# Optimization experiments

Measured on AMD Instinct MI355X. Metric: run time of the kernel, lower is better.

Reference implementation:

```python
import jax, jax.numpy as jnp
import numpy as np

IH, IW, HEADS, DIM_HEAD = 32, 32, 8, 48
N = IH * IW
SCALE = DIM_HEAD ** -0.5
EPS = 1e-5


def _relative_index():
    # static precompute of relative distance indices, shape [N, N] int32
    yy, xx = np.meshgrid(np.arange(IH), np.arange(IW), indexing='ij')
    coords = np.stack([yy.ravel(), xx.ravel()])  # [2, N]
    rel = coords[:, :, None] - coords[:, None, :]  # [2, N, N]
    dist = np.ceil(np.sqrt(rel[0] ** 2 + rel[1] ** 2)).astype(np.int32)
    return jnp.asarray(dist)

REL_INDEX = _relative_index()


def _layernorm(x, w, b):
    mu = jnp.mean(x, axis=-1, keepdims=True)
    var = jnp.var(x, axis=-1, keepdims=True)
    return (x - mu) * jax.lax.rsqrt(var + EPS) * w + b


def setup_inputs() -> dict:
    key = jax.random.key(0)
    ks = jax.random.split(key, 8)
    d, inner, hid = 384, HEADS * DIM_HEAD, 1536
    return {
        'x': jax.random.normal(ks[0], (16, IH, IW, d), jnp.float32),
        'ln1_w': jnp.ones((d,), jnp.float32),
        'ln1_b': jnp.zeros((d,), jnp.float32),
        'w_qkv': jax.random.normal(ks[1], (d, 3 * inner), jnp.float32) * (d ** -0.5),
        'bias_table': jax.random.normal(ks[2], (45, HEADS), jnp.float32) * 0.02,
        'w_out': jax.random.normal(ks[3], (inner, d), jnp.float32) * (inner ** -0.5),
        'b_out': jnp.zeros((d,), jnp.float32),
        'ln2_w': jnp.ones((d,), jnp.float32),
        'ln2_b': jnp.zeros((d,), jnp.float32),
        'w1': jax.random.normal(ks[4], (d, hid), jnp.float32) * (d ** -0.5),
        'b1': jnp.zeros((hid,), jnp.float32),
        'w2': jax.random.normal(ks[5], (hid, d), jnp.float32) * (hid ** -0.5),
        'b2': jnp.zeros((d,), jnp.float32),
    }


def reference(x, ln1_w, ln1_b, w_qkv, bias_table, w_out, b_out,
              ln2_w, ln2_b, w1, b1, w2, b2):
    b = x.shape[0]
    xt = x.reshape(b, N, -1)  # b (ih iw) c

    # --- attention branch (PreNorm) ---
    h = _layernorm(xt, ln1_w, ln1_b)
    qkv = h @ w_qkv  # [b, N, 3*inner]
    q, k, v = jnp.split(qkv, 3, axis=-1)
    q = q.reshape(b, N, HEADS, DIM_HEAD).transpose(0, 2, 1, 3)
    k = k.reshape(b, N, HEADS, DIM_HEAD).transpose(0, 2, 1, 3)
    v = v.reshape(b, N, HEADS, DIM_HEAD).transpose(0, 2, 1, 3)
    dots = jnp.einsum('bhnd,bhmd->bhnm', q, k) * SCALE
    rel_bias = bias_table[REL_INDEX]  # [N, N, heads] gather
    dots = dots + rel_bias.transpose(2, 0, 1)[None]  # [1, h, N, N]
    attn = jax.nn.softmax(dots, axis=-1)
    out = jnp.einsum('bhnm,bhmd->bhnd', attn, v)
    out = out.transpose(0, 2, 1, 3).reshape(b, N, HEADS * DIM_HEAD)
    out = out @ w_out + b_out
    xt = xt + out

    # --- FFN branch (PreNorm) ---
    h = _layernorm(xt, ln2_w, ln2_b)
    h = jax.nn.gelu(h @ w1 + b1, approximate=False) @ w2 + b2
    xt = xt + h
    return xt.reshape(x.shape)
```

## Files before the change

kernel.cpp:

```cpp
#include <hip/hip_runtime.h>
#include <hip/hip_bf16.h>
#include <math.h>

typedef __bf16 bf16;
typedef __bf16 bf16x8 __attribute__((ext_vector_type(8)));
typedef __bf16 bf16x4 __attribute__((ext_vector_type(4)));
typedef float  f32x4  __attribute__((ext_vector_type(4)));

#define D_MODEL 384
#define HID     1536
#define NSEQ    1024
#define ROWS    16384
#define HEADS   8
#define DH      48
#define SCALE   0.14433756729740643f
#define MFIX    8.0f
#define BTAB_N  3969
#define BTAB_P  3972
#define KVT     4608
#define QP_BH   (NSEQ * DH)
#define KP_BH   (16 * KVT)

__device__ __forceinline__ void gload16(const void* g, void* l) {
    __builtin_amdgcn_global_load_lds((const __attribute__((address_space(1))) void*)g,
                                     (__attribute__((address_space(3))) void*)l, 16, 0, 0);
}

__device__ __forceinline__ float fast_gelu(float x) {
    float u = 0.7978845608f * fmaf(0.044715f * x * x, x, x);
    float e = __expf(2.f * u);
    float t = 1.f - 2.f * __builtin_amdgcn_rcpf(e + 1.f);
    return 0.5f * x * (1.f + t);
}

__global__ __launch_bounds__(256)
void bias_prep_kernel(const float* __restrict__ bias_table, float* __restrict__ Btab)
{
    int idx = blockIdx.x * 256 + threadIdx.x;
    if (idx >= BTAB_N) return;
    int dy = idx / 63 - 31, dx = idx % 63 - 31;
    int s2 = dy * dy + dx * dx;
    int r = (int)ceilf(sqrtf((float)s2));
    while (r * r < s2) ++r;
    while (r > 0 && (r - 1) * (r - 1) >= s2) --r;
#pragma unroll
    for (int h = 0; h < HEADS; ++h)
        Btab[h * BTAB_P + idx] = bias_table[r * HEADS + h] - MFIX;
}

__global__ __launch_bounds__(256)
void pack_init_kernel(bf16* __restrict__ Kp, bf16* __restrict__ Vp)
{
    const int bid = blockIdx.x, tid = threadIdx.x;
    if (bid < 512) {
        int row = bid * 256 + tid;
        bf16x8 z = {};
        bf16* p = Kp + (size_t)row * 72 + 48;
        *(bf16x8*)(p) = z;  *(bf16x8*)(p + 8) = z;  *(bf16x8*)(p + 16) = z;
    } else {
        int idx = (bid - 512) * 256 + tid;
        int tile = idx >> 4, rr = idx & 15;
        bf16 o = (bf16)1.f;
        bf16x8 ones = {o, o, o, o, o, o, o, o};
        bf16* p = Vp + (size_t)tile * KVT + (48 + rr) * 72;
#pragma unroll
        for (int c = 0; c < 9; ++c) *(bf16x8*)(p + c * 8) = ones;
    }
}

__global__ __launch_bounds__(256)
void wtrans_kernel(const float* __restrict__ in, bf16* __restrict__ out, int K, int N)
{
    __shared__ float T[64][65];
    const int k0 = blockIdx.y * 64, n0 = blockIdx.x * 64;
    const int rr = threadIdx.x >> 4, rc = threadIdx.x & 15;
#pragma unroll
    for (int i = 0; i < 4; ++i) {
        float4 v = *(const float4*)(in + (size_t)(k0 + rr + i * 16) * N + n0 + rc * 4);
        T[rr + i * 16][rc * 4 + 0] = v.x;  T[rr + i * 16][rc * 4 + 1] = v.y;
        T[rr + i * 16][rc * 4 + 2] = v.z;  T[rr + i * 16][rc * 4 + 3] = v.w;
    }
    __syncthreads();
#pragma unroll
    for (int i = 0; i < 4; ++i) {
        int n = rr + i * 16, kc = rc * 4;
        bf16x4 o;
        o[0] = (bf16)T[kc + 0][n];  o[1] = (bf16)T[kc + 1][n];
        o[2] = (bf16)T[kc + 2][n];  o[3] = (bf16)T[kc + 3][n];
        *(bf16x4*)(out + (size_t)(n0 + n) * K + k0 + kc) = o;
    }
}

__global__ __launch_bounds__(64)
void ln_kernel(const float* __restrict__ x, const float* __restrict__ w,
               const float* __restrict__ b, bf16* __restrict__ out)
{
    int row  = blockIdx.x;
    int lane = threadIdx.x;
    const float* xr = x + (size_t)row * D_MODEL;

    float v[6], s = 0.f, ss = 0.f;
#pragma unroll
    for (int i = 0; i < 6; ++i) {
        v[i] = xr[lane + i * 64];
        s  += v[i];
        ss += v[i] * v[i];
    }
#pragma unroll
    for (int off = 32; off; off >>= 1) {
        s  += __shfl_xor(s,  off);
        ss += __shfl_xor(ss, off);
    }
    float mu   = s * (1.f / D_MODEL);
    float var  = ss * (1.f / D_MODEL) - mu * mu;
    float rstd = rsqrtf(var + 1e-5f);

    bf16* orow = out + (size_t)row * D_MODEL;
#pragma unroll
    for (int i = 0; i < 6; ++i) {
        int c = lane + i * 64;
        orow[c] = (bf16)((v[i] - mu) * rstd * w[c] + b[c]);
    }
}

template<int EPI, typename CT>
__global__ __launch_bounds__(256)
void gemm3_kernel(const bf16* __restrict__ A, const bf16* __restrict__ BT,
                  CT* __restrict__ C, const float* __restrict__ bias,
                  const float* __restrict__ res, int nxblk, int Nn, int K,
                  bf16* __restrict__ qp, bf16* __restrict__ kp, bf16* __restrict__ vp)
{
    __shared__ alignas(16) bf16 As[128][64];
    __shared__ alignas(16) bf16 Bs[128][64];

    const int bid  = blockIdx.x;
    const int xcd  = bid & 7;
    const int slot = bid >> 3;
    const int yy   = slot / nxblk;
    const int m0   = (yy * 8 + xcd) * 128;
    const int n0   = (slot - yy * nxblk) * 128;

    const int tid  = threadIdx.x;
    const int w    = tid >> 6;
    const int lane = tid & 63;
    const int quad = lane >> 4;
    const int l16  = lane & 15;

    const int srow = lane >> 3;
    const int scol = (lane & 7) * 8;

    f32x4 acc[4][4] = {};

    for (int kt = 0; kt < K; kt += 64) {
        __syncthreads();
#pragma unroll
        for (int c = 0; c < 4; ++c) {
            const int ch = w * 4 + c;
            gload16(A  + (size_t)(m0 + ch * 8 + srow) * K + kt + scol, &As[ch * 8][0]);
            gload16(BT + (size_t)(n0 + ch * 8 + srow) * K + kt + scol, &Bs[ch * 8][0]);
        }
        __syncthreads();

#pragma unroll
        for (int kk = 0; kk < 2; ++kk) {
            bf16x8 af[4], bfr[4];
#pragma unroll
            for (int mt = 0; mt < 4; ++mt)
                af[mt] = *(const bf16x8*)(&As[(w & 1) * 64 + mt * 16 + l16][kk * 32 + quad * 8]);
#pragma unroll
            for (int nt = 0; nt < 4; ++nt)
                bfr[nt] = *(const bf16x8*)(&Bs[(w >> 1) * 64 + nt * 16 + l16][kk * 32 + quad * 8]);
#pragma unroll
            for (int mt = 0; mt < 4; ++mt)
#pragma unroll
                for (int nt = 0; nt < 4; ++nt)
                    acc[mt][nt] = __builtin_amdgcn_mfma_f32_16x16x32_bf16(
                        af[mt], bfr[nt], acc[mt][nt], 0, 0, 0);
        }
    }

#pragma unroll
    for (int mt = 0; mt < 4; ++mt) {
#pragma unroll
        for (int nt = 0; nt < 4; ++nt) {
            const int c0 = n0 + (w >> 1) * 64 + nt * 16;
            const int c  = c0 + l16;
            float bi = (EPI == 1 || EPI == 2) ? bias[c] : 0.f;
#pragma unroll
            for (int r = 0; r < 4; ++r) {
                int row = m0 + (w & 1) * 64 + mt * 16 + quad * 4 + r;
                float v = acc[mt][nt][r] + bi;
                if (EPI == 1) {
                    v += res[(size_t)row * Nn + c];
                    C[(size_t)row * Nn + c] = (CT)v;
                } else if (EPI == 2) {
                    v = fast_gelu(v);
                    C[(size_t)row * Nn + c] = (CT)v;
                } else {
                    int b   = row >> 10, seq = row & 1023;
                    if (c0 < 384) {
                        int h = c / 48, d = c - h * 48;
                        qp[(size_t)(b * 8 + h) * QP_BH + seq * 48 + d] = (bf16)(v * SCALE);
                    } else if (c0 < 768) {
                        int ck = c - 384;
                        int h = ck / 48, d = ck - h * 48;
                        kp[(size_t)(b * 8 + h) * KP_BH + (seq >> 6) * KVT
                           + (seq & 63) * 72 + d] = (bf16)v;
                    } else {
                        int cv = c - 768;
                        int h = cv / 48, d = cv - h * 48;
                        vp[(size_t)(b * 8 + h) * KP_BH + (seq >> 6) * KVT
                           + d * 72 + (seq & 63)] = (bf16)v;
                    }
                }
            }
        }
    }
}

__global__ __launch_bounds__(256)
void attn_kernel(const bf16* __restrict__ Qp, const bf16* __restrict__ Kp,
                 const bf16* __restrict__ Vp, const float* __restrict__ Btab,
                 bf16* __restrict__ out)
{
    __shared__ alignas(16) bf16 Ks[64][72];
    __shared__ alignas(16) bf16 Vs[64][72];
    __shared__ alignas(16) bf16 Ps[4][2][16][72];
    __shared__ alignas(16) float B2f[BTAB_P];

    const int bid  = blockIdx.x;
    const int xcd  = bid & 7;
    const int slot = bid >> 3;
    const int qc   = slot & 7;
    const int bh   = (slot >> 3) * 8 + xcd;
    const int q0   = qc * 128;
    const int tid  = threadIdx.x;
    const int wave = tid >> 6;
    const int lane = tid & 63;
    const int quad = lane >> 4;
    const int l16  = lane & 15;
    const int b    = bh >> 3, h = bh & 7;

    {
        const char* src = (const char*)(Btab + h * BTAB_P);
#pragma unroll
        for (int it = 0; it < 4; ++it) {
            int off = it * 4096 + tid * 16;
            if (off < BTAB_P * 4)
                gload16(src + off, (char*)B2f + it * 4096 + wave * 1024);
        }
    }

    bf16x8 qf0[2], qf1[2];
    int pi[2];
#pragma unroll
    for (int s = 0; s < 2; ++s) {
        int qrow = q0 + s * 64 + wave * 16 + l16;
        const bf16* qptr = Qp + (size_t)bh * QP_BH + qrow * 48;
        qf0[s] = *(const bf16x8*)(qptr + quad * 8);
#pragma unroll
        for (int c = 0; c < 8; ++c) qf1[s][c] = (bf16)0.f;
        if (quad < 2) qf1[s] = *(const bf16x8*)(qptr + 32 + quad * 8);
        pi[s] = (qrow >> 5) * 63 + (qrow & 31) + 31 * 63 + 31;
    }

    f32x4 o_acc[2][4] = {};

    for (int t = 0; t < 16; ++t) {
        const int n0 = t * 64;
        const bf16* kbase = Kp + (size_t)(bh * 16 + t) * KVT;
        const bf16* vbase = Vp + (size_t)(bh * 16 + t) * KVT;
        __syncthreads();
        for (int i = wave; i < 9; i += 4) {
            gload16(kbase + i * 512 + lane * 8, (bf16*)Ks + i * 512);
            gload16(vbase + i * 512 + lane * 8, (bf16*)Vs + i * 512);
        }
        __syncthreads();

        f32x4 sa[2][4] = {};
#pragma unroll
        for (int nt = 0; nt < 4; ++nt) {
            bf16x8 a0 = *(const bf16x8*)(&Ks[nt * 16 + l16][quad * 8]);
            bf16x8 a1 = *(const bf16x8*)(&Ks[nt * 16 + l16][32 + quad * 8]);
#pragma unroll
            for (int s = 0; s < 2; ++s) {
                sa[s][nt] = __builtin_amdgcn_mfma_f32_16x16x32_bf16(a0, qf0[s], sa[s][nt], 0, 0, 0);
                sa[s][nt] = __builtin_amdgcn_mfma_f32_16x16x32_bf16(a1, qf1[s], sa[s][nt], 0, 0, 0);
            }
        }

#pragma unroll
        for (int s = 0; s < 2; ++s)
#pragma unroll
            for (int nt = 0; nt < 4; ++nt) {
                const int j0 = n0 + nt * 16 + quad * 4;
                const int ib = pi[s] - ((j0 >> 5) * 63 + (j0 & 31));
                bf16x4 pk;
#pragma unroll
                for (int r = 0; r < 4; ++r)
                    pk[r] = (bf16)__expf(sa[s][nt][r] + B2f[ib - r]);
                *(bf16x4*)(&Ps[wave][s][l16][nt * 16 + quad * 4]) = pk;
            }

#pragma unroll
        for (int kk = 0; kk < 2; ++kk) {
            bf16x8 vf[4];
#pragma unroll
            for (int d = 0; d < 4; ++d)
                vf[d] = *(const bf16x8*)(&Vs[d * 16 + l16][kk * 32 + quad * 8]);
#pragma unroll
            for (int s = 0; s < 2; ++s) {
                bf16x8 pf = *(const bf16x8*)(&Ps[wave][s][l16][kk * 32 + quad * 8]);
#pragma unroll
                for (int d = 0; d < 4; ++d)
                    o_acc[s][d] = __builtin_amdgcn_mfma_f32_16x16x32_bf16(
                        pf, vf[d], o_acc[s][d], 0, 0, 0);
            }
        }
    }

#pragma unroll
    for (int s = 0; s < 2; ++s)
#pragma unroll
        for (int r = 0; r < 4; ++r) {
            float inv = 1.f / o_acc[s][3][r];
            int row = q0 + s * 64 + wave * 16 + quad * 4 + r;
            bf16* orow = out + ((size_t)b * NSEQ + row) * D_MODEL + h * DH;
#pragma unroll
            for (int d = 0; d < 3; ++d)
                orow[d * 16 + l16] = (bf16)(o_acc[s][d][r] * inv);
        }
}

extern "C" void kernel_launch(void* const* d_in, const int* in_sizes, int n_in,
                              void* d_out, int out_size, void* d_ws, size_t ws_size,
                              hipStream_t stream)
{
    const float* x          = (const float*)d_in[0];
    const float* ln1_w      = (const float*)d_in[1];
    const float* ln1_b      = (const float*)d_in[2];
    const float* w_qkv      = (const float*)d_in[3];
    const float* bias_table = (const float*)d_in[4];
    const float* w_out      = (const float*)d_in[5];
    const float* b_out      = (const float*)d_in[6];
    const float* ln2_w      = (const float*)d_in[7];
    const float* ln2_b      = (const float*)d_in[8];
    const float* w1         = (const float*)d_in[9];
    const float* b1         = (const float*)d_in[10];
    const float* w2         = (const float*)d_in[11];
    const float* b2         = (const float*)d_in[12];
    float* out = (float*)d_out;

    bf16* regA  = (bf16*)d_ws;
    bf16* Qpack = regA;
    bf16* Kpack = regA + 6291456;
    bf16* Vpack = regA + 15728640;
    bf16* regB  = regA + (size_t)ROWS * HID;
    bf16* wqkvT = regB + (size_t)ROWS * D_MODEL;
    bf16* woutT = wqkvT + 1152 * 384;
    bf16* w1T   = woutT + 384 * 384;
    bf16* w2T   = w1T + 1536 * 384;
    float* Btab = (float*)(w2T + 384 * 1536);
    float* x1   = out;

    bias_prep_kernel<<<(BTAB_N + 255) / 256, 256, 0, stream>>>(bias_table, Btab);
    pack_init_kernel<<<640, 256, 0, stream>>>(Kpack, Vpack);
    wtrans_kernel<<<dim3(1152 / 64, 384 / 64), 256, 0, stream>>>(w_qkv, wqkvT, 384, 1152);
    wtrans_kernel<<<dim3(384 / 64, 384 / 64), 256, 0, stream>>>(w_out, woutT, 384, 384);
    wtrans_kernel<<<dim3(1536 / 64, 384 / 64), 256, 0, stream>>>(w1, w1T, 384, 1536);
    wtrans_kernel<<<dim3(384 / 64, 1536 / 64), 256, 0, stream>>>(w2, w2T, 1536, 384);

    ln_kernel<<<ROWS, 64, 0, stream>>>(x, ln1_w, ln1_b, regB);
    gemm3_kernel<3, bf16><<<(1152 / 128) * (ROWS / 128), 256, 0, stream>>>(
        regB, wqkvT, (bf16*)nullptr, nullptr, nullptr, 1152 / 128, 1152, D_MODEL,
        Qpack, Kpack, Vpack);
    attn_kernel<<<1024, 256, 0, stream>>>(Qpack, Kpack, Vpack, Btab, regB);
    gemm3_kernel<1, float><<<(D_MODEL / 128) * (ROWS / 128), 256, 0, stream>>>(
        regB, woutT, x1, b_out, x, D_MODEL / 128, D_MODEL, D_MODEL,
        nullptr, nullptr, nullptr);
    ln_kernel<<<ROWS, 64, 0, stream>>>(x1, ln2_w, ln2_b, regB);
    gemm3_kernel<2, bf16><<<(HID / 128) * (ROWS / 128), 256, 0, stream>>>(
        regB, w1T, regA, b1, nullptr, HID / 128, HID, D_MODEL,
        nullptr, nullptr, nullptr);
    gemm3_kernel<1, float><<<(D_MODEL / 128) * (ROWS / 128), 256, 0, stream>>>(
        regA, w2T, out, b2, x1, D_MODEL / 128, D_MODEL, HID,
        nullptr, nullptr, nullptr);
}
```

Before: 329.7 us.

## Stage QKV epilogue through LDS for vector stores; shrink attention LDS footprint

The QKV GEMM epilogue now writes the accumulator tile to shared memory and then emits 16-byte vectorized stores into the packed Q/K/V layouts, transposing through LDS for V. This replaces scattered 2-byte global writes. The attention kernel stores the relative-position bias table as bf16 and reuses a single P buffer per wave, which cuts LDS use and may raise occupancy. Risks include lower precision in the bias and removal of the MFIX max-shift of -8 applied before exp, which could change overflow behavior.

```diff
diff --git a/kernel.cpp b/kernel.cpp
--- a/kernel.cpp
+++ b/kernel.cpp
@@ -14,9 +14,8 @@
 #define HEADS   8
 #define DH      48
 #define SCALE   0.14433756729740643f
-#define MFIX    8.0f
 #define BTAB_N  3969
-#define BTAB_P  3972
+#define BTAB_PB 3976
 #define KVT     4608
 #define QP_BH   (NSEQ * DH)
 #define KP_BH   (16 * KVT)
@@ -34,7 +33,7 @@
 }
 
 __global__ __launch_bounds__(256)
-void bias_prep_kernel(const float* __restrict__ bias_table, float* __restrict__ Btab)
+void bias_prep_kernel(const float* __restrict__ bias_table, bf16* __restrict__ Btab)
 {
     int idx = blockIdx.x * 256 + threadIdx.x;
     if (idx >= BTAB_N) return;
@@ -45,7 +44,7 @@
     while (r > 0 && (r - 1) * (r - 1) >= s2) --r;
 #pragma unroll
     for (int h = 0; h < HEADS; ++h)
-        Btab[h * BTAB_P + idx] = bias_table[r * HEADS + h] - MFIX;
+        Btab[h * BTAB_PB + idx] = (bf16)bias_table[r * HEADS + h];
 }
 
 __global__ __launch_bounds__(256)
@@ -130,8 +129,10 @@
                   const float* __restrict__ res, int nxblk, int Nn, int K,
                   bf16* __restrict__ qp, bf16* __restrict__ kp, bf16* __restrict__ vp)
 {
-    __shared__ alignas(16) bf16 As[128][64];
-    __shared__ alignas(16) bf16 Bs[128][64];
+    constexpr int SMEM = (EPI == 3) ? (128 * 136 * 2) : 32768;
+    __shared__ alignas(16) char smem[SMEM];
+    bf16 (*As)[64] = (bf16(*)[64])smem;
+    bf16 (*Bs)[64] = (bf16(*)[64])(smem + 16384);
 
     const int bid  = blockIdx.x;
     const int xcd  = bid & 7;
@@ -179,40 +180,68 @@
         }
     }
 
-#pragma unroll
-    for (int mt = 0; mt < 4; ++mt) {
-#pragma unroll
-        for (int nt = 0; nt < 4; ++nt) {
-            const int c0 = n0 + (w >> 1) * 64 + nt * 16;
-            const int c  = c0 + l16;
-            float bi = (EPI == 1 || EPI == 2) ? bias[c] : 0.f;
-#pragma unroll
-            for (int r = 0; r < 4; ++r) {
-                int row = m0 + (w & 1) * 64 + mt * 16 + quad * 4 + r;
-                float v = acc[mt][nt][r] + bi;
-                if (EPI == 1) {
-                    v += res[(size_t)row * Nn + c];
+    if (EPI != 3) {
+#pragma unroll
+        for (int mt = 0; mt < 4; ++mt) {
+#pragma unroll
+            for (int nt = 0; nt < 4; ++nt) {
+                int c = n0 + (w >> 1) * 64 + nt * 16 + l16;
+                float bi = bias ? bias[c] : 0.f;
+#pragma unroll
+                for (int r = 0; r < 4; ++r) {
+                    int row = m0 + (w & 1) * 64 + mt * 16 + quad * 4 + r;
+                    float v = acc[mt][nt][r] + bi;
+                    if (EPI == 1) v += res[(size_t)row * Nn + c];
+                    if (EPI == 2) v = fast_gelu(v);
                     C[(size_t)row * Nn + c] = (CT)v;
-                } else if (EPI == 2) {
-                    v = fast_gelu(v);
-                    C[(size_t)row * Nn + c] = (CT)v;
-                } else {
-                    int b   = row >> 10, seq = row & 1023;
-                    if (c0 < 384) {
-                        int h = c / 48, d = c - h * 48;
-                        qp[(size_t)(b * 8 + h) * QP_BH + seq * 48 + d] = (bf16)(v * SCALE);
-                    } else if (c0 < 768) {
-                        int ck = c - 384;
-                        int h = ck / 48, d = ck - h * 48;
-                        kp[(size_t)(b * 8 + h) * KP_BH + (seq >> 6) * KVT
-                           + (seq & 63) * 72 + d] = (bf16)v;
-                    } else {
-                        int cv = c - 768;
-                        int h = cv / 48, d = cv - h * 48;
-                        vp[(size_t)(b * 8 + h) * KP_BH + (seq >> 6) * KVT
-                           + d * 72 + (seq & 63)] = (bf16)v;
-                    }
                 }
+            }
+        }
+    } else {
+        bf16 (*Ts)[136] = (bf16(*)[136])smem;
+        const float mult = (n0 < 384) ? SCALE : 1.f;
+        __syncthreads();
+#pragma unroll
+        for (int mt = 0; mt < 4; ++mt)
+#pragma unroll
+            for (int nt = 0; nt < 4; ++nt)
+#pragma unroll
+                for (int r = 0; r < 4; ++r)
+                    Ts[(w & 1) * 64 + mt * 16 + quad * 4 + r]
+                      [(w >> 1) * 64 + nt * 16 + l16] = (bf16)(acc[mt][nt][r] * mult);
+        __syncthreads();
+
+        const int b = m0 >> 10, seqbase = m0 & 1023;
+        if (n0 < 768) {
+            const bool isQ = (n0 < 384);
+#pragma unroll
+            for (int it = 0; it < 8; ++it) {
+                int task = it * 256 + tid;
+                int sq = task >> 4, ch = task & 15;
+                int c0 = n0 + ch * 8 - (isQ ? 0 : 384);
+                int h = c0 / 48, d0 = c0 - h * 48;
+                bf16x8 v = *(const bf16x8*)(&Ts[sq][ch * 8]);
+                int seq = seqbase + sq;
+                if (isQ)
+                    *(bf16x8*)(qp + (size_t)(b * 8 + h) * QP_BH + seq * 48 + d0) = v;
+                else
+                    *(bf16x8*)(kp + (size_t)(b * 8 + h) * KP_BH + (seq >> 6) * KVT
+                               + (seq & 63) * 72 + d0) = v;
+            }
+        } else {
+#pragma unroll
+            for (int it = 0; it < 8; ++it) {
+                int task = it * 256 + tid;
+                int colL = task & 127, kc = task >> 7;
+                int key0 = kc * 8;
+                int cv = n0 + colL - 768;
+                int h = cv / 48, d = cv - h * 48;
+                bf16x8 v;
+#pragma unroll
+                for (int j = 0; j < 8; ++j) v[j] = Ts[key0 + j][colL];
+                int seq = seqbase + key0;
+                *(bf16x8*)(vp + (size_t)(b * 8 + h) * KP_BH + (seq >> 6) * KVT
+                           + d * 72 + (seq & 63)) = v;
             }
         }
     }
@@ -220,13 +249,13 @@
 
 __global__ __launch_bounds__(256)
 void attn_kernel(const bf16* __restrict__ Qp, const bf16* __restrict__ Kp,
-                 const bf16* __restrict__ Vp, const float* __restrict__ Btab,
+                 const bf16* __restrict__ Vp, const bf16* __restrict__ Btab,
                  bf16* __restrict__ out)
 {
     __shared__ alignas(16) bf16 Ks[64][72];
     __shared__ alignas(16) bf16 Vs[64][72];
-    __shared__ alignas(16) bf16 Ps[4][2][16][72];
-    __shared__ alignas(16) float B2f[BTAB_P];
+    __shared__ alignas(16) bf16 Ps[4][16][72];
+    __shared__ alignas(16) bf16 B2b[BTAB_PB];
 
     const int bid  = blockIdx.x;
     const int xcd  = bid & 7;
@@ -242,12 +271,12 @@
     const int b    = bh >> 3, h = bh & 7;
 
     {
-        const char* src = (const char*)(Btab + h * BTAB_P);
-#pragma unroll
-        for (int it = 0; it < 4; ++it) {
+        const char* src = (const char*)(Btab + h * BTAB_PB);
+#pragma unroll
+        for (int it = 0; it < 2; ++it) {
             int off = it * 4096 + tid * 16;
-            if (off < BTAB_P * 4)
-                gload16(src + off, (char*)B2f + it * 4096 + wave * 1024);
+            if (off < BTAB_PB * 2)
+                gload16(src + off, (char*)B2b + it * 4096 + wave * 1024);
         }
     }
 
@@ -290,7 +319,7 @@
         }
 
 #pragma unroll
-        for (int s = 0; s < 2; ++s)
+        for (int s = 0; s < 2; ++s) {
 #pragma unroll
             for (int nt = 0; nt < 4; ++nt) {
                 const int j0 = n0 + nt * 16 + quad * 4;
@@ -298,23 +327,18 @@
                 bf16x4 pk;
 #pragma unroll
                 for (int r = 0; r < 4; ++r)
-                    pk[r] = (bf16)__expf(sa[s][nt][r] + B2f[ib - r]);
-                *(bf16x4*)(&Ps[wave][s][l16][nt * 16 + quad * 4]) = pk;
-            }
-
-#pragma unroll
-        for (int kk = 0; kk < 2; ++kk) {
-            bf16x8 vf[4];
-#pragma unroll
-            for (int d = 0; d < 4; ++d)
-                vf[d] = *(const bf16x8*)(&Vs[d * 16 + l16][kk * 32 + quad * 8]);
-#pragma unroll
-            for (int s = 0; s < 2; ++s) {
-                bf16x8 pf = *(const bf16x8*)(&Ps[wave][s][l16][kk * 32 + quad * 8]);
-#pragma unroll
-                for (int d = 0; d < 4; ++d)
+                    pk[r] = (bf16)__expf(sa[s][nt][r] + (float)B2b[ib - r]);
+                *(bf16x4*)(&Ps[wave][l16][nt * 16 + quad * 4]) = pk;
+            }
+#pragma unroll
+            for (int kk = 0; kk < 2; ++kk) {
+                bf16x8 pf = *(const bf16x8*)(&Ps[wave][l16][kk * 32 + quad * 8]);
+#pragma unroll
+                for (int d = 0; d < 4; ++d) {
+                    bf16x8 vf = *(const bf16x8*)(&Vs[d * 16 + l16][kk * 32 + quad * 8]);
                     o_acc[s][d] = __builtin_amdgcn_mfma_f32_16x16x32_bf16(
-                        pf, vf[d], o_acc[s][d], 0, 0, 0);
+                        pf, vf, o_acc[s][d], 0, 0, 0);
+                }
             }
         }
     }
@@ -360,7 +384,7 @@
     bf16* woutT = wqkvT + 1152 * 384;
     bf16* w1T   = woutT + 384 * 384;
     bf16* w2T   = w1T + 1536 * 384;
-    float* Btab = (float*)(w2T + 384 * 1536);
+    bf16* Btab  = w2T + 384 * 1536;
     float* x1   = out;
 
     bias_prep_kernel<<<(BTAB_N + 255) / 256, 256, 0, stream>>>(bias_table, Btab);
```

After: 370.0 us. +12.2%, slower.
